# Optimization experiments

Hardware: AMD Instinct MI355X
Metric: run time of the kernel (lower is better)

## Reference

```python
import jax, jax.numpy as jnp
import numpy as np

D_MODEL = 1024

def setup_inputs() -> dict:
    key = jax.random.key(0)
    kx, kq, kk, kv, ko = jax.random.split(key, 5)
    B, S, D = 4, 2048, D_MODEL
    scale = 1.0 / np.sqrt(D)
    return {
        "x": jax.random.normal(kx, (B, S, D), dtype=jnp.float32),
        "w_q": jax.random.normal(kq, (D, D), dtype=jnp.float32) * scale,
        "w_k": jax.random.normal(kk, (D, D), dtype=jnp.float32) * scale,
        "w_v": jax.random.normal(kv, (D, D), dtype=jnp.float32) * scale,
        "w_out": jax.random.normal(ko, (D, D), dtype=jnp.float32) * scale,
    }

def reference(x, w_q, w_k, w_v, w_out):
    # Single-head attention: projections are Linear(d_model,d_model,bias=False).
    # torch Linear computes x @ W.T; weights here stored as [out,in].
    Q = jnp.einsum('bsd,ed->bse', x, w_q)
    K = jnp.einsum('bsd,ed->bse', x, w_k)
    V = jnp.einsum('bsd,ed->bse', x, w_v)
    d_model = x.shape[-1]
    scores = jnp.einsum('bqe,bke->bqk', Q, K) / jnp.sqrt(jnp.float32(d_model))
    attn = jax.nn.softmax(scores, axis=-1)
    out = jnp.einsum('bqk,bke->bqe', attn, V)
    return jnp.einsum('bse,oe->bso', out, w_out)
```

## Files before the change

### kernel.cpp

```cpp
#include <hip/hip_runtime.h>

typedef unsigned int uint;
typedef unsigned short ushort;
typedef __bf16 bf16x8 __attribute__((ext_vector_type(8)));
typedef float f32x4 __attribute__((ext_vector_type(4)));

__device__ __forceinline__ ushort f2bf(float v) {
    uint u = __builtin_bit_cast(uint, v);
    u += 0x7fffu + ((u >> 16) & 1u);
    return (ushort)(u >> 16);
}

__device__ __forceinline__ void storeval(float* p, float v)  { *p = v; }
__device__ __forceinline__ void storeval(ushort* p, float v) { *p = f2bf(v); }

#define GLDS(g, l) __builtin_amdgcn_global_load_lds( \
    (const __attribute__((address_space(1))) uint*)(g), \
    (__attribute__((address_space(3))) uint*)(l), 16, 0, 0)

#define VMW(N)  asm volatile("s_waitcnt vmcnt(" #N ")" ::: "memory")
#define SBAR()  asm volatile("s_barrier" ::: "memory")

__device__ __forceinline__ void stage_half(const ushort* __restrict__ src, int ld,
                                           int halfrow, char* ldsbase, int tid)
{
#pragma unroll
    for (int i = 0; i < 2; i++) {
        const int byte = i * 8192 + tid * 16;
        const int row  = byte >> 7;
        const int slot = (byte >> 4) & 7;
        const int srcs = slot ^ (row & 7);
        GLDS(src + (long long)(halfrow + row) * ld + srcs * 8,
             ldsbase + halfrow * 128 + byte);
    }
}

__device__ __forceinline__ bf16x8 ldf(const char* base, int rbase, int ks,
                                      int lrow, int lquad)
{
    const int r    = rbase + lrow;
    const int slot = ((ks << 2) + lquad) ^ (r & 7);
    return *(const bf16x8*)(base + r * 128 + slot * 16);
}

#define RD_A(BASE, ROFF) \
    _Pragma("unroll") for (int m_ = 0; m_ < 4; m_++) \
    _Pragma("unroll") for (int k_ = 0; k_ < 2; k_++) \
        af[m_][k_] = ldf(BASE, (ROFF) + m_ * 16, k_, lrow, lquad);

#define RD_B(DST, BASE, ROFF) \
    _Pragma("unroll") for (int n_ = 0; n_ < 2; n_++) \
    _Pragma("unroll") for (int k_ = 0; k_ < 2; k_++) \
        DST[n_][k_] = ldf(BASE, (ROFF) + n_ * 16, k_, lrow, lquad);

#define QUAD(MOFF, NOFF, B) \
    __builtin_amdgcn_s_setprio(1); \
    _Pragma("unroll") for (int m_ = 0; m_ < 4; m_++) \
    _Pragma("unroll") for (int n_ = 0; n_ < 2; n_++) \
    _Pragma("unroll") for (int k_ = 0; k_ < 2; k_++) \
        acc[(MOFF) + m_][(NOFF) + n_] = __builtin_amdgcn_mfma_f32_16x16x32_bf16( \
            af[m_][k_], B[n_][k_], acc[(MOFF) + m_][(NOFF) + n_], 0, 0, 0); \
    __builtin_amdgcn_s_setprio(0);

template<bool EXP>
__global__ __launch_bounds__(512, 2)
void gemm256_8ph(const ushort* __restrict__ A, int lda, long long bsA,
                 const ushort* __restrict__ Bt, int ldb, long long bsB,
                 ushort* __restrict__ C, int ldc, long long bsC,
                 int K, float scale, float* __restrict__ Zp)
{
    __shared__ char smem[131072];
    char* A0 = smem;
    char* A1 = smem + 32768;
    char* B0 = smem + 65536;
    char* B1 = smem + 98304;

    const int tid   = threadIdx.x;
    const int lane  = tid & 63;
    const int wave  = tid >> 6;
    const int wr    = wave >> 2;
    const int wc    = wave & 3;
    const int lrow  = lane & 15;
    const int lquad = lane >> 4;
    const long long b = blockIdx.z;

    const ushort* Ag = A  + b * bsA + (long long)blockIdx.y * 256 * lda;
    const ushort* Bg = Bt + b * bsB + (long long)blockIdx.x * 256 * ldb;
    ushort*       Cg = C  + b * bsC + (long long)blockIdx.y * 256 * ldc
                           + (long long)blockIdx.x * 256;

    f32x4 acc[8][4] = {};
    bf16x8 af[4][2], bl[2][2], bh[2][2];

    const int nk    = K >> 6;
    const int nIter = nk >> 1;

    stage_half(Ag,      lda, 0,   A0, tid);
    stage_half(Bg,      ldb, 0,   B0, tid);
    stage_half(Bg,      ldb, 128, B0, tid);
    stage_half(Ag,      lda, 128, A0, tid);
    stage_half(Ag + 64, lda, 0,   A1, tid);
    stage_half(Bg + 64, ldb, 0,   B1, tid);
    stage_half(Bg + 64, ldb, 128, B1, tid);
    VMW(6); SBAR();

    for (int i = 0; i < nIter - 1; ++i) {
        const ushort* An1 = Ag + (2 * i + 1) * 64;
        const ushort* An2 = Ag + (2 * i + 2) * 64;
        const ushort* Bn2 = Bg + (2 * i + 2) * 64;
        const ushort* An3 = Ag + (2 * i + 3) * 64;
        const ushort* Bn3 = Bg + (2 * i + 3) * 64;

        RD_A(A0, wr * 64); RD_B(bl, B0, wc * 32);
        stage_half(An1, lda, 128, A1, tid);
        SBAR(); QUAD(0, 0, bl); SBAR();

        RD_B(bh, B0, 128 + wc * 32);
        stage_half(An2, lda, 0, A0, tid);
        SBAR(); QUAD(0, 2, bh); SBAR();

        RD_A(A0, 128 + wr * 64);
        stage_half(Bn2, ldb, 0, B0, tid);
        SBAR(); QUAD(4, 0, bl); SBAR();

        stage_half(Bn2, ldb, 128, B0, tid);
        SBAR(); QUAD(4, 2, bh); VMW(6); SBAR();

        RD_A(A1, wr * 64); RD_B(bl, B1, wc * 32);
        stage_half(An2, lda, 128, A0, tid);
        SBAR(); QUAD(0, 0, bl); SBAR();

        RD_B(bh, B1, 128 + wc * 32);
        stage_half(An3, lda, 0, A1, tid);
        SBAR(); QUAD(0, 2, bh); SBAR();

        RD_A(A1, 128 + wr * 64);
        stage_half(Bn3, ldb, 0, B1, tid);
        SBAR(); QUAD(4, 0, bl); SBAR();

        stage_half(Bn3, ldb, 128, B1, tid);
        SBAR(); QUAD(4, 2, bh); VMW(6); SBAR();
    }

    {
        const ushort* An1 = Ag + (nk - 1) * 64;

        RD_A(A0, wr * 64); RD_B(bl, B0, wc * 32);
        stage_half(An1, lda, 128, A1, tid);
        SBAR(); QUAD(0, 0, bl); SBAR();

        RD_B(bh, B0, 128 + wc * 32);
        SBAR(); QUAD(0, 2, bh); SBAR();

        RD_A(A0, 128 + wr * 64);
        SBAR(); QUAD(4, 0, bl); SBAR();

        SBAR(); QUAD(4, 2, bh); VMW(0); SBAR();

        RD_A(A1, wr * 64); RD_B(bl, B1, wc * 32);
        SBAR(); QUAD(0, 0, bl); SBAR();

        RD_B(bh, B1, 128 + wc * 32);
        SBAR(); QUAD(0, 2, bh); SBAR();

        RD_A(A1, 128 + wr * 64);
        SBAR(); QUAD(4, 0, bl); SBAR();

        SBAR(); QUAD(4, 2, bh);
    }

#pragma unroll
    for (int m = 0; m < 8; m++) {
        const int row = (m >> 2) * 128 + wr * 64 + (m & 3) * 16 + lquad * 4;
        float rs[4] = {0.f, 0.f, 0.f, 0.f};
#pragma unroll
        for (int n = 0; n < 4; n++) {
            const int col = (n >> 1) * 128 + wc * 32 + (n & 1) * 16 + lrow;
#pragma unroll
            for (int j = 0; j < 4; j++) {
                float v = acc[m][n][j];
                if (EXP) {
                    float e = __expf(v * scale);
                    rs[j] += e;
                    Cg[(long long)(row + j) * ldc + col] = f2bf(e);
                } else {
                    Cg[(long long)(row + j) * ldc + col] = f2bf(v);
                }
            }
        }
        if (EXP) {
#pragma unroll
            for (int j = 0; j < 4; j++) {
                float s = rs[j];
                s += __shfl_xor(s, 1);
                s += __shfl_xor(s, 2);
                s += __shfl_xor(s, 4);
                s += __shfl_xor(s, 8);
                rs[j] = s;
            }
            if (lrow == 0) {
                const long long zi = ((long long)b * 32 + blockIdx.x * 4 + wc) * 2048
                                   + (long long)blockIdx.y * 256 + row;
#pragma unroll
                for (int j = 0; j < 4; j++) Zp[zi + j] = rs[j];
            }
        }
    }
}

__global__ __launch_bounds__(512, 2)
void pv3(const ushort* __restrict__ A, int lda, long long bsA,
         const ushort* __restrict__ Bt, int ldb, long long bsB,
         float* __restrict__ C, int ldc, long long bsC,
         int K, const float* __restrict__ Zp)
{
    __shared__ char smem[147456];
    __shared__ float zbuf[128];

    const int tid   = threadIdx.x;
    const int lane  = tid & 63;
    const int wave  = tid >> 6;
    const int wr    = wave >> 2;
    const int wc    = wave & 3;
    const int lrow  = lane & 15;
    const int lquad = lane >> 4;
    const long long b = blockIdx.z;

    if (tid < 128) {
        const float* p = Zp + b * 32 * 2048 + (long long)blockIdx.y * 128 + tid;
        float s = 0.f;
#pragma unroll
        for (int i = 0; i < 32; i++) s += p[i * 2048];
        zbuf[tid] = 1.0f / s;
    }
    __syncthreads();

    const ushort* Ag = A  + b * bsA + (long long)blockIdx.y * 128 * lda;
    const ushort* Bg = Bt + b * bsB + (long long)blockIdx.x * 256 * ldb;
    float*        Cg = C  + b * bsC + (long long)blockIdx.y * 128 * ldc
                           + (long long)blockIdx.x * 256;

    f32x4 acc[4][4] = {};
    bf16x8 af[4][2], bl[2][2], bh[2][2];

    const int nk = K >> 6;

#define STAGE_TILE(T, I) do { \
        stage_half(Ag + (T) * 64, lda, 0,   smem + (I) * 16384,         tid); \
        stage_half(Bg + (T) * 64, ldb, 0,   smem + 49152 + (I) * 32768, tid); \
        stage_half(Bg + (T) * 64, ldb, 128, smem + 49152 + (I) * 32768, tid); \
    } while (0)

    STAGE_TILE(0, 0);
    STAGE_TILE(1, 1);
    VMW(6); SBAR();

    int cur = 0;
    for (int t = 0; t < nk; ++t) {
        const char* lAc = smem + cur * 16384;
        const char* lBc = smem + 49152 + cur * 32768;

        RD_A(lAc, wr * 64);
        RD_B(bl, lBc, wc * 32);
        RD_B(bh, lBc, 128 + wc * 32);

        if (t + 2 < nk) {
            int nxt = cur + 2; if (nxt >= 3) nxt -= 3;
            STAGE_TILE(t + 2, nxt);
        }

        QUAD(0, 0, bl);
        QUAD(0, 2, bh);

        if (t + 1 < nk) {
            if (t + 2 < nk) { VMW(6); } else { VMW(0); }
            SBAR();
        }
        cur = (cur == 2) ? 0 : cur + 1;
    }
#undef STAGE_TILE

#pragma unroll
    for (int m = 0; m < 4; m++) {
        const int row = wr * 64 + m * 16 + lquad * 4;
        f32x4 z4 = *(const f32x4*)&zbuf[row];
#pragma unroll
        for (int n = 0; n < 4; n++) {
            const int col = (n >> 1) * 128 + wc * 32 + (n & 1) * 16 + lrow;
#pragma unroll
            for (int j = 0; j < 4; j++)
                storeval(&Cg[(long long)(row + j) * ldc + col], acc[m][n][j] * z4[j]);
        }
    }
}

__global__ __launch_bounds__(256)
void wgemm_splitk(const ushort* __restrict__ A0, const ushort* __restrict__ B0,
                  const ushort* __restrict__ A1, const ushort* __restrict__ B1,
                  float* __restrict__ P)
{
    __shared__ ushort lA[128 * 64];
    __shared__ ushort lB[128 * 64];

    const int z    = blockIdx.z;
    const int pair = z >> 1;
    const int ksl  = z & 1;

    const ushort* A  = pair ? A1 : A0;
    const ushort* Bt = pair ? B1 : B0;

    const int tid  = threadIdx.x;
    const int lane = tid & 63;
    const int wave = tid >> 6;
    const int wr   = wave >> 1;
    const int wc   = wave & 1;

    A  += (long long)blockIdx.y * 128 * 1024 + ksl * 512;
    Bt += (long long)blockIdx.x * 128 * 1024 + ksl * 512;
    float* Pg = P + (long long)z * 1048576
                  + (long long)blockIdx.y * 128 * 1024 + (long long)blockIdx.x * 128;

    f32x4 acc[4][4] = {};
    const int byte_base = wave * 1024 + lane * 16;

    for (int kt = 0; kt < 512; kt += 64) {
#pragma unroll
        for (int i = 0; i < 4; i++) {
            const int byte = i * 4096 + byte_base;
            const int row  = byte >> 7;
            const int k0   = (byte & 127) >> 1;
            GLDS(A  + (long long)row * 1024 + kt + k0, (char*)lA + byte);
            GLDS(Bt + (long long)row * 1024 + kt + k0, (char*)lB + byte);
        }
        __syncthreads();

#pragma unroll
        for (int ks = 0; ks < 2; ks++) {
            bf16x8 af2[4], bf2[4];
#pragma unroll
            for (int m = 0; m < 4; m++)
                af2[m] = *(const bf16x8*)&lA[(wr * 64 + m * 16 + (lane & 15)) * 64 + ks * 32 + (lane >> 4) * 8];
#pragma unroll
            for (int n = 0; n < 4; n++)
                bf2[n] = *(const bf16x8*)&lB[(wc * 64 + n * 16 + (lane & 15)) * 64 + ks * 32 + (lane >> 4) * 8];
#pragma unroll
            for (int m = 0; m < 4; m++)
#pragma unroll
                for (int n = 0; n < 4; n++)
                    acc[m][n] = __builtin_amdgcn_mfma_f32_16x16x32_bf16(af2[m], bf2[n], acc[m][n], 0, 0, 0);
        }
        __syncthreads();
    }

    const int r0 = wr * 64 + (lane >> 4) * 4;
    const int c0 = wc * 64 + (lane & 15);
#pragma unroll
    for (int m = 0; m < 4; m++)
#pragma unroll
        for (int n = 0; n < 4; n++)
#pragma unroll
            for (int j = 0; j < 4; j++)
                Pg[(long long)(r0 + m * 16 + j) * 1024 + c0 + n * 16] = acc[m][n][j];
}

__global__ __launch_bounds__(256)
void wreduce(const float* __restrict__ P, ushort* __restrict__ W2)
{
    const int i = blockIdx.x * 256 + threadIdx.x;
    const int pair = i >> 18;
    const int off  = (i & 262143) * 4;
    const float* base = P + (long long)pair * 2097152 + off;
    float4 s = *(const float4*)(base);
    float4 v = *(const float4*)(base + 1048576);
    s.x += v.x; s.y += v.y; s.z += v.z; s.w += v.w;
    ushort o[4] = { f2bf(s.x), f2bf(s.y), f2bf(s.z), f2bf(s.w) };
    *(uint2*)&W2[(long long)pair * 1048576 + off] = *(const uint2*)&o[0];
}

__global__ __launch_bounds__(256)
void f32_to_bf16_vec(const float* __restrict__ in, ushort* __restrict__ out, int n4)
{
    int i = blockIdx.x * 256 + threadIdx.x;
    if (i >= n4) return;
    float4 v = ((const float4*)in)[i];
    ushort o[4] = { f2bf(v.x), f2bf(v.y), f2bf(v.z), f2bf(v.w) };
    *(uint2*)&out[(size_t)i * 4] = *(const uint2*)&o[0];
}

__global__ __launch_bounds__(256)
void wprep(const float* __restrict__ s0, const float* __restrict__ s1,
           const float* __restrict__ s2, const float* __restrict__ s3,
           ushort* __restrict__ wT, ushort* __restrict__ wo_bf)
{
    __shared__ float t[64][65];
    const int z = blockIdx.z;
    const int k0 = blockIdx.y * 64, j0 = blockIdx.x * 64;
    const int r = threadIdx.x >> 2;
    const int c = (threadIdx.x & 3) * 16;

    if (z == 3) {
        const float* p = s3 + (size_t)(k0 + r) * 1024 + j0 + c;
        float4 a = *(const float4*)(p);
        float4 bq = *(const float4*)(p + 4);
        float4 cc = *(const float4*)(p + 8);
        float4 d = *(const float4*)(p + 12);
        ushort o[16] = { f2bf(a.x), f2bf(a.y), f2bf(a.z), f2bf(a.w),
                         f2bf(bq.x), f2bf(bq.y), f2bf(bq.z), f2bf(bq.w),
                         f2bf(cc.x), f2bf(cc.y), f2bf(cc.z), f2bf(cc.w),
                         f2bf(d.x), f2bf(d.y), f2bf(d.z), f2bf(d.w) };
        ushort* q = wo_bf + (size_t)(k0 + r) * 1024 + j0 + c;
        *(uint4*)q       = *(const uint4*)&o[0];
        *(uint4*)(q + 8) = *(const uint4*)&o[8];
        return;
    }

    const float* src = (z == 0) ? s0 : (z == 1) ? s1 : s2;
    ushort* dst = wT + (size_t)z * 1048576;

    const float* p = src + (size_t)(k0 + r) * 1024 + j0 + c;
#pragma unroll
    for (int j = 0; j < 16; j++) t[r][c + j] = p[j];
    __syncthreads();

    ushort o[16];
#pragma unroll
    for (int j = 0; j < 16; j++) o[j] = f2bf(t[c + j][r]);
    ushort* q = dst + (size_t)(j0 + r) * 1024 + k0 + c;
    *(uint4*)q       = *(const uint4*)&o[0];
    *(uint4*)(q + 8) = *(const uint4*)&o[8];
}

__global__ __launch_bounds__(256)
void transpose_v(const ushort* __restrict__ V, int ldv, long long bsV,
                 ushort* __restrict__ Vt)
{
    __shared__ ushort t[64][65];
    const int b = blockIdx.z;
    const ushort* src = V  + (size_t)b * bsV;
    ushort*       dst = Vt + (size_t)b * 1024 * 2048;
    const int e0 = blockIdx.x * 64;
    const int k0 = blockIdx.y * 64;
    const int r = threadIdx.x >> 2;
    const int c = (threadIdx.x & 3) * 16;

    const ushort* p = &src[(size_t)(k0 + r) * ldv + e0 + c];
    ushort vals[16];
    *(uint4*)&vals[0] = *(const uint4*)p;
    *(uint4*)&vals[8] = *(const uint4*)(p + 8);
#pragma unroll
    for (int j = 0; j < 16; j++) t[r][c + j] = vals[j];
    __syncthreads();

    ushort o[16];
#pragma unroll
    for (int j = 0; j < 16; j++) o[j] = t[c + j][r];
    ushort* q = &dst[(size_t)(e0 + r) * 2048 + k0 + c];
    *(uint4*)q       = *(const uint4*)&o[0];
    *(uint4*)(q + 8) = *(const uint4*)&o[8];
}

extern "C" void kernel_launch(void* const* d_in, const int* in_sizes, int n_in,
                              void* d_out, int out_size, void* d_ws, size_t ws_size,
                              hipStream_t stream)
{
    const float* x  = (const float*)d_in[0];
    const float* wq = (const float*)d_in[1];
    const float* wk = (const float*)d_in[2];
    const float* wv = (const float*)d_in[3];
    const float* wo = (const float*)d_in[4];
    float* out = (float*)d_out;

    char* ws = (char*)d_ws;
    ushort* xb    = (ushort*)(ws);
    ushort* W2    = (ushort*)(ws + 16777216);
    ushort* wT    = (ushort*)(ws + 20971520);
    ushort* wo_bf = (ushort*)(ws + 27262976);
    ushort* TVw   = (ushort*)(ws + 29360128);
    ushort* Vtb   = (ushort*)(ws + 62914560);
    ushort* E     = (ushort*)(ws + 79691776);
    float*  Pp    = (float*)(ws + 79691776);
    float*  Zp    = (float*)(ws + 113246208);

    ushort* wqT = wT;
    ushort* wkT = wT + 1048576;
    ushort* wvT = wT + 2097152;

    f32_to_bf16_vec<<<8192, 256, 0, stream>>>(x, xb, 2097152);
    wprep<<<dim3(16, 16, 4), 256, 0, stream>>>(wq, wk, wv, wo, wT, wo_bf);

    wgemm_splitk<<<dim3(8, 8, 4), 256, 0, stream>>>(wkT, wqT, wo_bf, wvT, Pp);
    wreduce<<<2048, 256, 0, stream>>>(Pp, W2);

    gemm256_8ph<false><<<dim3(8, 32, 1), 512, 0, stream>>>(
        xb, 1024, 0, W2, 1024, 0, TVw, 2048, 0, 1024, 1.f, nullptr);

    transpose_v<<<dim3(16, 32, 4), 256, 0, stream>>>(TVw + 1024, 2048, 2048LL * 2048, Vtb);

    gemm256_8ph<true><<<dim3(8, 8, 4), 512, 0, stream>>>(
        TVw, 2048, 2048LL * 2048, xb, 1024, 2048LL * 1024,
        E, 2048, 2048LL * 2048, 1024, 0.03125f, Zp);

    pv3<<<dim3(4, 16, 4), 512, 0, stream>>>(
        E, 2048, 2048LL * 2048, Vtb, 2048, 1024LL * 2048,
        out, 1024, 2048LL * 1024, 2048, Zp);
}
```

Baseline: 164.5 us.

## Fuse V transpose into projection GEMM epilogue and merge prep kernels

The projection GEMM now writes the V half of its output directly in transposed layout (Vt) from registers, so the separate transpose_v kernel and the wide TVw buffer are no longer needed. The T half goes to a narrower buffer that the scores GEMM reads. The x conversion and weight prep kernels are also merged into one launch to cut launch overhead. The transposed epilogue writes 8-byte chunks strided by 2048 elements, which coalesces poorly and may cost bandwidth.

```diff
diff --git a/kernel.cpp b/kernel.cpp
--- a/kernel.cpp
+++ b/kernel.cpp
@@ -67,7 +67,8 @@
 void gemm256_8ph(const ushort* __restrict__ A, int lda, long long bsA,
                  const ushort* __restrict__ Bt, int ldb, long long bsB,
                  ushort* __restrict__ C, int ldc, long long bsC,
-                 int K, float scale, float* __restrict__ Zp)
+                 int K, float scale, float* __restrict__ Zp,
+                 ushort* __restrict__ Vt)
 {
     __shared__ char smem[131072];
     char* A0 = smem;
@@ -86,8 +87,6 @@
 
     const ushort* Ag = A  + b * bsA + (long long)blockIdx.y * 256 * lda;
     const ushort* Bg = Bt + b * bsB + (long long)blockIdx.x * 256 * ldb;
-    ushort*       Cg = C  + b * bsC + (long long)blockIdx.y * 256 * ldc
-                           + (long long)blockIdx.x * 256;
 
     f32x4 acc[8][4] = {};
     bf16x8 af[4][2], bl[2][2], bh[2][2];
@@ -168,6 +167,28 @@
 
         SBAR(); QUAD(4, 2, bh);
     }
+
+    if (!EXP && Vt != nullptr && blockIdx.x >= 4) {
+        const int b2 = (int)(blockIdx.y >> 3);
+        const int kb = (int)(blockIdx.y & 7) * 256;
+        ushort* Vg = Vt + (long long)b2 * 1024 * 2048
+                   + (long long)(blockIdx.x - 4) * 256 * 2048 + kb;
+#pragma unroll
+        for (int m = 0; m < 8; m++) {
+            const int row = (m >> 2) * 128 + wr * 64 + (m & 3) * 16 + lquad * 4;
+#pragma unroll
+            for (int n = 0; n < 4; n++) {
+                const int col = (n >> 1) * 128 + wc * 32 + (n & 1) * 16 + lrow;
+                ushort o[4] = { f2bf(acc[m][n][0]), f2bf(acc[m][n][1]),
+                                f2bf(acc[m][n][2]), f2bf(acc[m][n][3]) };
+                *(uint2*)&Vg[(long long)col * 2048 + row] = *(const uint2*)&o[0];
+            }
+        }
+        return;
+    }
+
+    ushort* Cg = C + b * bsC + (long long)blockIdx.y * 256 * ldc
+                   + (long long)blockIdx.x * 256;
 
 #pragma unroll
     for (int m = 0; m < 8; m++) {
@@ -378,36 +399,35 @@
 }
 
 __global__ __launch_bounds__(256)
-void f32_to_bf16_vec(const float* __restrict__ in, ushort* __restrict__ out, int n4)
-{
-    int i = blockIdx.x * 256 + threadIdx.x;
-    if (i >= n4) return;
-    float4 v = ((const float4*)in)[i];
-    ushort o[4] = { f2bf(v.x), f2bf(v.y), f2bf(v.z), f2bf(v.w) };
-    *(uint2*)&out[(size_t)i * 4] = *(const uint2*)&o[0];
-}
-
-__global__ __launch_bounds__(256)
-void wprep(const float* __restrict__ s0, const float* __restrict__ s1,
-           const float* __restrict__ s2, const float* __restrict__ s3,
-           ushort* __restrict__ wT, ushort* __restrict__ wo_bf)
+void prep(const float* __restrict__ x, ushort* __restrict__ xb,
+          const float* __restrict__ s0, const float* __restrict__ s1,
+          const float* __restrict__ s2, const float* __restrict__ s3,
+          ushort* __restrict__ wT, ushort* __restrict__ wo_bf)
 {
     __shared__ float t[64][65];
-    const int z = blockIdx.z;
-    const int k0 = blockIdx.y * 64, j0 = blockIdx.x * 64;
+
+    if (blockIdx.x < 8192) {
+        const int i = blockIdx.x * 256 + threadIdx.x;
+        float4 v = ((const float4*)x)[i];
+        ushort o[4] = { f2bf(v.x), f2bf(v.y), f2bf(v.z), f2bf(v.w) };
+        *(uint2*)&xb[(size_t)i * 4] = *(const uint2*)&o[0];
+        return;
+    }
+
+    const int idx = blockIdx.x - 8192;
+    const int z   = idx >> 8;
+    const int r2  = idx & 255;
+    const int by  = r2 >> 4;
+    const int bx  = r2 & 15;
+    const int k0 = by * 64, j0 = bx * 64;
     const int r = threadIdx.x >> 2;
     const int c = (threadIdx.x & 3) * 16;
 
     if (z == 3) {
         const float* p = s3 + (size_t)(k0 + r) * 1024 + j0 + c;
-        float4 a = *(const float4*)(p);
-        float4 bq = *(const float4*)(p + 4);
-        float4 cc = *(const float4*)(p + 8);
-        float4 d = *(const float4*)(p + 12);
-        ushort o[16] = { f2bf(a.x), f2bf(a.y), f2bf(a.z), f2bf(a.w),
-                         f2bf(bq.x), f2bf(bq.y), f2bf(bq.z), f2bf(bq.w),
-                         f2bf(cc.x), f2bf(cc.y), f2bf(cc.z), f2bf(cc.w),
-                         f2bf(d.x), f2bf(d.y), f2bf(d.z), f2bf(d.w) };
+        ushort o[16];
+#pragma unroll
+        for (int j = 0; j < 16; j++) o[j] = f2bf(p[j]);
         ushort* q = wo_bf + (size_t)(k0 + r) * 1024 + j0 + c;
         *(uint4*)q       = *(const uint4*)&o[0];
         *(uint4*)(q + 8) = *(const uint4*)&o[8];
@@ -426,35 +446,6 @@
 #pragma unroll
     for (int j = 0; j < 16; j++) o[j] = f2bf(t[c + j][r]);
     ushort* q = dst + (size_t)(j0 + r) * 1024 + k0 + c;
-    *(uint4*)q       = *(const uint4*)&o[0];
-    *(uint4*)(q + 8) = *(const uint4*)&o[8];
-}
-
-__global__ __launch_bounds__(256)
-void transpose_v(const ushort* __restrict__ V, int ldv, long long bsV,
-                 ushort* __restrict__ Vt)
-{
-    __shared__ ushort t[64][65];
-    const int b = blockIdx.z;
-    const ushort* src = V  + (size_t)b * bsV;
-    ushort*       dst = Vt + (size_t)b * 1024 * 2048;
-    const int e0 = blockIdx.x * 64;
-    const int k0 = blockIdx.y * 64;
-    const int r = threadIdx.x >> 2;
-    const int c = (threadIdx.x & 3) * 16;
-
-    const ushort* p = &src[(size_t)(k0 + r) * ldv + e0 + c];
-    ushort vals[16];
-    *(uint4*)&vals[0] = *(const uint4*)p;
-    *(uint4*)&vals[8] = *(const uint4*)(p + 8);
-#pragma unroll
-    for (int j = 0; j < 16; j++) t[r][c + j] = vals[j];
-    __syncthreads();
-
-    ushort o[16];
-#pragma unroll
-    for (int j = 0; j < 16; j++) o[j] = t[c + j][r];
-    ushort* q = &dst[(size_t)(e0 + r) * 2048 + k0 + c];
     *(uint4*)q       = *(const uint4*)&o[0];
     *(uint4*)(q + 8) = *(const uint4*)&o[8];
 }
@@ -475,30 +466,27 @@
     ushort* W2    = (ushort*)(ws + 16777216);
     ushort* wT    = (ushort*)(ws + 20971520);
     ushort* wo_bf = (ushort*)(ws + 27262976);
-    ushort* TVw   = (ushort*)(ws + 29360128);
-    ushort* Vtb   = (ushort*)(ws + 62914560);
-    ushort* E     = (ushort*)(ws + 79691776);
-    float*  Pp    = (float*)(ws + 79691776);
-    float*  Zp    = (float*)(ws + 113246208);
+    ushort* Tbuf  = (ushort*)(ws + 29360128);
+    ushort* Vtb   = (ushort*)(ws + 46137344);
+    ushort* E     = (ushort*)(ws + 62914560);
+    float*  Pp    = (float*)(ws + 62914560);
+    float*  Zp    = (float*)(ws + 96468992);
 
     ushort* wqT = wT;
     ushort* wkT = wT + 1048576;
     ushort* wvT = wT + 2097152;
 
-    f32_to_bf16_vec<<<8192, 256, 0, stream>>>(x, xb, 2097152);
-    wprep<<<dim3(16, 16, 4), 256, 0, stream>>>(wq, wk, wv, wo, wT, wo_bf);
+    prep<<<9216, 256, 0, stream>>>(x, xb, wq, wk, wv, wo, wT, wo_bf);
 
     wgemm_splitk<<<dim3(8, 8, 4), 256, 0, stream>>>(wkT, wqT, wo_bf, wvT, Pp);
     wreduce<<<2048, 256, 0, stream>>>(Pp, W2);
 
     gemm256_8ph<false><<<dim3(8, 32, 1), 512, 0, stream>>>(
-        xb, 1024, 0, W2, 1024, 0, TVw, 2048, 0, 1024, 1.f, nullptr);
-
-    transpose_v<<<dim3(16, 32, 4), 256, 0, stream>>>(TVw + 1024, 2048, 2048LL * 2048, Vtb);
+        xb, 1024, 0, W2, 1024, 0, Tbuf, 1024, 0, 1024, 1.f, nullptr, Vtb);
 
     gemm256_8ph<true><<<dim3(8, 8, 4), 512, 0, stream>>>(
-        TVw, 2048, 2048LL * 2048, xb, 1024, 2048LL * 1024,
-        E, 2048, 2048LL * 2048, 1024, 0.03125f, Zp);
+        Tbuf, 1024, 2048LL * 1024, xb, 1024, 2048LL * 1024,
+        E, 2048, 2048LL * 2048, 1024, 0.03125f, Zp, nullptr);
 
     pv3<<<dim3(4, 16, 4), 512, 0, stream>>>(
         E, 2048, 2048LL * 2048, Vtb, 2048, 1024LL * 2048,
```

Result: faster. 155.0 us (median of 2 runs) (-5.8%).
